# Kernel tuning notes

Measured on AMD Instinct MI355X. Metric: run time of the kernel, lower is better.

The kernel has to match this reference:

```python
import jax, jax.numpy as jnp
import numpy as np

GAMMA = 0.01      # rbf gamma (init kwarg)
C = 10            # n_classes (len(nv))
NV = 500          # support vectors per class (equal segments)
# all (i, j) class pairs with i < j, in the original nested-loop order
PAIRS = np.array([(i, j) for i in range(C) for j in range(i + 1, C)], dtype=np.int32)
I_IDX = jnp.asarray(PAIRS[:, 0])  # [45]
J_IDX = jnp.asarray(PAIRS[:, 1])  # [45]


def setup_inputs() -> dict:
    key = jax.random.key(0)
    k1, k2, k3, k4 = jax.random.split(key, 4)
    x = jax.random.normal(k1, (8192, 256), dtype=jnp.float32)
    sv = jax.random.normal(k2, (5000, 256), dtype=jnp.float32)
    a = jax.random.normal(k3, (C - 1, 5000), dtype=jnp.float32) * 0.1  # dual coefs
    b = jax.random.normal(k4, (45,), dtype=jnp.float32) * 0.1          # intercepts per pair
    return {"x": x, "sv": sv, "a": a, "b": b}


def reference(x, sv, a, b):
    # RBF kernel matrix: k[n, s] = exp(-gamma * ||x_n - sv_s||^2)
    x_norm = jnp.sum(x * x, axis=1)[:, None]            # [N, 1]
    sv_norm = jnp.sum(sv * sv, axis=1)[None, :]         # [1, SV]
    k = jnp.exp(-GAMMA * (x_norm + sv_norm) + 2.0 * GAMMA * (x @ sv.T))  # [N, SV]

    N = x.shape[0]
    kr = k.reshape(N, C, NV)           # per-class SV segments
    ar = a.reshape(C - 1, C, NV)       # dual coef rows, segmented the same way
    # T[n, r, c] = sum_m a[r, segment c, m] * k[n, segment c, m]
    # (fuses every inner Python loop of the original into one contraction)
    T = jnp.einsum('ncm,rcm->nrc', kr, ar)              # [N, C-1, C]

    # decision for pair (i, j): a[i, seg j] . k_seg_j + a[j-1, seg i] . k_seg_i + b
    c = T[:, I_IDX, J_IDX] + T[:, J_IDX - 1, I_IDX] + b[None, :]  # [N, 45]

    # pairwise voting: winner i if c > 0 else j; class id = mode of votes
    votes = jnp.where(c > 0, I_IDX[None, :], J_IDX[None, :])      # [N, 45] int32
    counts = jnp.sum(jax.nn.one_hot(votes, C, dtype=jnp.float32), axis=1)  # [N, C]
    # argmax picks the smallest class index on ties, matching torch.mode
    class_ids = jnp.argmax(counts, axis=1).astype(jnp.int32)
    return (class_ids, class_ids)
```

## Files before the change

### kernel.cpp

```cpp
#include <hip/hip_runtime.h>
#include <hip/hip_fp16.h>
#include <cmath>


#define GAMMA 0.01f
constexpr int N  = 8192;
constexpr int D  = 256;
constexpr int S  = 5000;
constexpr int C  = 10;
constexpr int NV = 500;
constexpr int R  = 9;
constexpr int SPAD = 5120;

constexpr int ROW_BLOCKS = (N + S) / 4;
constexpr int A_BLOCKS   = (16 * SPAD) / 256;

typedef _Float16 f16x8 __attribute__((ext_vector_type(8)));
typedef _Float16 f16x4 __attribute__((ext_vector_type(4)));
typedef float    f32x4 __attribute__((ext_vector_type(4)));

__device__ __forceinline__ void gload16(const void* g, void* l) {
    __builtin_amdgcn_global_load_lds(
        (const __attribute__((address_space(1))) void*)g,
        (__attribute__((address_space(3))) void*)l, 16, 0, 0);
}

__global__ __launch_bounds__(256) void prep_kernel(const float* __restrict__ x,
                                                   const float* __restrict__ sv,
                                                   const float* __restrict__ a,
                                                   _Float16* __restrict__ xth,
                                                   _Float16* __restrict__ xtl,
                                                   _Float16* __restrict__ sh,
                                                   _Float16* __restrict__ sl,
                                                   float* __restrict__ xn,
                                                   _Float16* __restrict__ ah,
                                                   _Float16* __restrict__ al,
                                                   float* __restrict__ svnp) {
    if (blockIdx.x >= ROW_BLOCKS) {
        int idx = (blockIdx.x - ROW_BLOCKS) * 256 + threadIdx.x;
        int r = idx / SPAD, col = idx - r * SPAD;
        int cls = col >> 9, j = col & 511;
        int s = cls * NV + ((j < NV) ? j : NV - 1);
        float av = (r < R && j < NV) ? a[(size_t)r * S + s] : 0.0f;
        _Float16 h = (_Float16)av;
        ah[idx] = h;
        al[idx] = (_Float16)((av - (float)h) * 4096.0f);
        return;
    }
    int gid  = blockIdx.x * blockDim.x + threadIdx.x;
    int wid  = gid >> 6;
    int lane = gid & 63;
    bool isx = wid < N;
    int  r   = isx ? wid : wid - N;
    const float* row = isx ? (x + (size_t)r * D) : (sv + (size_t)r * D);
    float4 v = reinterpret_cast<const float4*>(row)[lane];
    float s = v.x * v.x + v.y * v.y + v.z * v.z + v.w * v.w;
#pragma unroll
    for (int off = 32; off > 0; off >>= 1) s += __shfl_xor(s, off, 64);
    float vv[4] = {v.x, v.y, v.z, v.w};
    f16x4 h, l;
#pragma unroll
    for (int k = 0; k < 4; ++k) {
        _Float16 hi = (_Float16)vv[k];
        h[k] = hi;
        l[k] = (_Float16)((vv[k] - (float)hi) * 4096.0f);
    }
    if (isx) {
        size_t xt = (((size_t)(r >> 4) * 8 + (lane >> 3)) * 4 + ((lane >> 1) & 3)) * 128
                  + (size_t)(r & 15) * 8 + (lane & 1) * 4;
        *(f16x4*)(xth + xt) = h;
        *(f16x4*)(xtl + xt) = l;
    } else {
        size_t o = (size_t)r * D + lane * 4;
        *(f16x4*)(sh + o) = h;
        *(f16x4*)(sl + o) = l;
    }
    if (lane == 0) {
        if (isx) {
            xn[r] = s;
        } else {
            int cls = r / NV, j = r - cls * NV;
            svnp[cls * 512 + j] = s;
            if (j == NV - 1)
                for (int p = NV; p < 512; ++p) svnp[cls * 512 + p] = s;
        }
    }
}

__global__ __launch_bounds__(128, 3) void svc_gemm(const _Float16* __restrict__ xth,
                                                   const _Float16* __restrict__ xtl,
                                                   const _Float16* __restrict__ sh,
                                                   const _Float16* __restrict__ sl,
                                                   const _Float16* __restrict__ ahp,
                                                   const _Float16* __restrict__ alp,
                                                   const float* __restrict__ xnorm,
                                                   const float* __restrict__ svnp,
                                                   float* __restrict__ T) {
    __shared__ _Float16 SVs[2][2][64 * 32];

    const int tid  = threadIdx.x;
    const int n0   = blockIdx.x * 64;
    const int cls  = blockIdx.y;
    const int w    = tid >> 6;
    const int lane = tid & 63;
    const int lx   = lane & 15;
    const int quad = lane >> 4;

    float xnr[2];
#pragma unroll
    for (int nt = 0; nt < 2; ++nt)
        xnr[nt] = xnorm[n0 + w * 32 + nt * 16 + lx];

    int svoff[4];
#pragma unroll
    for (int mt = 0; mt < 4; ++mt) {
        int row = mt * 16 + lx;
        svoff[mt] = row * 32 + ((quad - (row >> 1)) & 3) * 8;
    }

    const int arow = tid >> 2, ag = tid & 3;
    const int sg   = (ag + (arow >> 1)) & 3;
    const int segend = cls * NV + NV - 1;
    const int ldsw = w * 512;

    auto stage = [&](int ph, int buf) {
        const int ch = ph >> 3, kb = ph & 7;
        const size_t koff = (size_t)(kb * 32 + sg * 8);
        const int svbase = cls * NV + ch * 64;
        int svr0 = svbase + arow;      if (svr0 > segend) svr0 = segend;
        int svr1 = svbase + arow + 32; if (svr1 > segend) svr1 = segend;
        const size_t go0 = (size_t)svr0 * D + koff;
        const size_t go1 = (size_t)svr1 * D + koff;
        gload16(sh + go0, &SVs[buf][0][ldsw]);
        gload16(sl + go0, &SVs[buf][1][ldsw]);
        gload16(sh + go1, &SVs[buf][0][1024 + ldsw]);
        gload16(sl + go1, &SVs[buf][1][1024 + ldsw]);
    };

    const int pn0 = blockIdx.x * 4 + w * 2;
    const size_t xq = (size_t)quad * 128 + (size_t)lx * 8;
    f16x8 pBE[2][2], pBO[2][2];
    auto loadB = [&](f16x8 (&dst)[2][2], int kb) {
        const size_t o0 = ((size_t)(pn0 * 8 + kb) * 4) * 128 + xq;
        const size_t o1 = ((size_t)((pn0 + 1) * 8 + kb) * 4) * 128 + xq;
        dst[0][0] = *(const f16x8*)(xth + o0);
        dst[1][0] = *(const f16x8*)(xtl + o0);
        dst[0][1] = *(const f16x8*)(xth + o1);
        dst[1][1] = *(const f16x8*)(xtl + o1);
    };

    f32x4 accM[4][2], accC[4][2];
#pragma unroll
    for (int mt = 0; mt < 4; ++mt)
#pragma unroll
        for (int nt = 0; nt < 2; ++nt) {
            accM[mt][nt] = (f32x4){0.f, 0.f, 0.f, 0.f};
            accC[mt][nt] = (f32x4){0.f, 0.f, 0.f, 0.f};
        }
    f32x4 accO[2], accOC[2];
#pragma unroll
    for (int nt = 0; nt < 2; ++nt) {
        accO[nt]  = (f32x4){0.f, 0.f, 0.f, 0.f};
        accOC[nt] = (f32x4){0.f, 0.f, 0.f, 0.f};
    }

    auto compute = [&](int buf, const f16x8 (&pB)[2][2]) {
        f16x8 Am[2][4];
#pragma unroll
        for (int mt = 0; mt < 4; ++mt) {
            Am[0][mt] = *(const f16x8*)(&SVs[buf][0][svoff[mt]]);
            Am[1][mt] = *(const f16x8*)(&SVs[buf][1][svoff[mt]]);
        }
        __builtin_amdgcn_s_setprio(1);
#pragma unroll
        for (int mt = 0; mt < 4; ++mt)
#pragma unroll
            for (int nt = 0; nt < 2; ++nt) {
                accM[mt][nt] = __builtin_amdgcn_mfma_f32_16x16x32_f16(
                    Am[0][mt], pB[0][nt], accM[mt][nt], 0, 0, 0);
                accC[mt][nt] = __builtin_amdgcn_mfma_f32_16x16x32_f16(
                    Am[0][mt], pB[1][nt], accC[mt][nt], 0, 0, 0);
                accC[mt][nt] = __builtin_amdgcn_mfma_f32_16x16x32_f16(
                    Am[1][mt], pB[0][nt], accC[mt][nt], 0, 0, 0);
            }
        __builtin_amdgcn_s_setprio(0);
    };

    auto epilogue = [&](int ch) {
        const int mbase = cls * 512 + ch * 64;
#pragma unroll
        for (int mt = 0; mt < 4; ++mt) {
            const size_t ao = (size_t)lx * SPAD + mbase + mt * 16 + quad * 4;
            f16x4 afh = *(const f16x4*)(ahp + ao);
            f16x4 afl = *(const f16x4*)(alp + ao);
            float4 sn4 = *(const float4*)(svnp + mbase + mt * 16 + quad * 4);
#pragma unroll
            for (int nt = 0; nt < 2; ++nt) {
                f16x4 bh, bl;
#pragma unroll
                for (int reg = 0; reg < 4; ++reg) {
                    float dot = accM[mt][nt][reg]
                              + accC[mt][nt][reg] * (1.0f / 4096.0f);
                    float e  = fmaf(2.0f * GAMMA, dot,
                                    -GAMMA * (xnr[nt] + sn4[reg]));
                    float kv = __expf(e);
                    _Float16 h = (_Float16)kv;
                    bh[reg] = h;
                    bl[reg] = (_Float16)((kv - (float)h) * 4096.0f);
                }
                accO[nt]  = __builtin_amdgcn_mfma_f32_16x16x16f16(
                    afh, bh, accO[nt], 0, 0, 0);
                accOC[nt] = __builtin_amdgcn_mfma_f32_16x16x16f16(
                    afh, bl, accOC[nt], 0, 0, 0);
                accOC[nt] = __builtin_amdgcn_mfma_f32_16x16x16f16(
                    afl, bh, accOC[nt], 0, 0, 0);
                accM[mt][nt] = (f32x4){0.f, 0.f, 0.f, 0.f};
                accC[mt][nt] = (f32x4){0.f, 0.f, 0.f, 0.f};
            }
        }
    };

    stage(0, 0);
    loadB(pBE, 0);

    for (int it = 0; it < 32; ++it) {
        asm volatile("s_waitcnt lgkmcnt(0)" ::: "memory");
        asm volatile("s_waitcnt vmcnt(4)" ::: "memory");
        __builtin_amdgcn_s_barrier();
        asm volatile("" ::: "memory");
        stage(2 * it + 1, 1);
        loadB(pBO, (2 * it + 1) & 7);
        compute(0, pBE);
        asm volatile("s_waitcnt lgkmcnt(0)" ::: "memory");
        asm volatile("s_waitcnt vmcnt(4)" ::: "memory");
        __builtin_amdgcn_s_barrier();
        asm volatile("" ::: "memory");
        if (it < 31) {
            stage(2 * it + 2, 0);
            loadB(pBE, (2 * it + 2) & 7);
        }
        compute(1, pBO);
        if ((it & 3) == 3) epilogue(it >> 2);
    }

#pragma unroll
    for (int nt = 0; nt < 2; ++nt)
#pragma unroll
        for (int reg = 0; reg < 4; ++reg) {
            int r = quad * 4 + reg;
            if (r < R) {
                int n = n0 + w * 32 + nt * 16 + lx;
                T[(size_t)(r * 10 + cls) * N + n] =
                    accO[nt][reg] + accOC[nt][reg] * (1.0f / 4096.0f);
            }
        }
}

__global__ __launch_bounds__(256) void vote_kernel(const float* __restrict__ T,
                                                   const float* __restrict__ b,
                                                   int* __restrict__ out) {
    int n = blockIdx.x * blockDim.x + threadIdx.x;
    if (n >= N) return;
    float tv[90];
#pragma unroll
    for (int i = 0; i < 90; ++i) tv[i] = T[(size_t)i * N + n];
    int counts[C];
#pragma unroll
    for (int k = 0; k < C; ++k) counts[k] = 0;
    int p = 0;
#pragma unroll
    for (int i = 0; i < C; ++i) {
#pragma unroll
        for (int j = i + 1; j < C; ++j) {
            float c = tv[i * 10 + j] + tv[(j - 1) * 10 + i] + b[p];
            if (c > 0.f) counts[i]++; else counts[j]++;
            ++p;
        }
    }
    int best = 0;
#pragma unroll
    for (int k = 1; k < C; ++k)
        if (counts[k] > counts[best]) best = k;
    out[n]     = best;
    out[N + n] = best;
}

extern "C" void kernel_launch(void* const* d_in, const int* in_sizes, int n_in,
                              void* d_out, int out_size, void* d_ws, size_t ws_size,
                              hipStream_t stream) {
    const float* x  = (const float*)d_in[0];
    const float* sv = (const float*)d_in[1];
    const float* a  = (const float*)d_in[2];
    const float* b  = (const float*)d_in[3];
    int* out = (int*)d_out;

    char* wp = (char*)d_ws;
    _Float16* xth = (_Float16*)wp; wp += (size_t)N * D * 2;
    _Float16* xtl = (_Float16*)wp; wp += (size_t)N * D * 2;
    _Float16* sh  = (_Float16*)wp; wp += (size_t)S * D * 2;
    _Float16* sl  = (_Float16*)wp; wp += (size_t)S * D * 2;
    float* xnorm  = (float*)wp;    wp += (size_t)N * 4;
    _Float16* ahp = (_Float16*)wp; wp += (size_t)16 * SPAD * 2;
    _Float16* alp = (_Float16*)wp; wp += (size_t)16 * SPAD * 2;
    float* svnp   = (float*)wp;    wp += (size_t)SPAD * 4;
    float* T      = (float*)wp;

    {
        prep_kernel<<<ROW_BLOCKS + A_BLOCKS, 256, 0, stream>>>(
            x, sv, a, xth, xtl, sh, sl, xnorm, ahp, alp, svnp);
    }
    {
        dim3 grid(N / 64, C);
        svc_gemm<<<grid, 128, 0, stream>>>(xth, xtl, sh, sl, ahp, alp,
                                           xnorm, svnp, T);
    }
    {
        vote_kernel<<<N / 256, 256, 0, stream>>>(T, b, out);
    }
}
```

Measured before the change: 169.9 us.

## Use single-wave GEMM blocks to drop barriers in the pipelined loop

Shrinks each svc_gemm block to one 64-lane wave covering 32 rows, so the LDS double-buffer no longer needs s_barrier between phases and relies only on vmcnt/lgkmcnt waits. The wave now issues all eight SV tile loads itself, and the grid doubles. This removes cross-wave synchronisation stalls at the cost of loading each SV tile twice as often from global/L2 memory.

```diff
diff --git a/kernel.cpp b/kernel.cpp
--- a/kernel.cpp
+++ b/kernel.cpp
@@ -87,29 +87,27 @@
     }
 }
 
-__global__ __launch_bounds__(128, 3) void svc_gemm(const _Float16* __restrict__ xth,
-                                                   const _Float16* __restrict__ xtl,
-                                                   const _Float16* __restrict__ sh,
-                                                   const _Float16* __restrict__ sl,
-                                                   const _Float16* __restrict__ ahp,
-                                                   const _Float16* __restrict__ alp,
-                                                   const float* __restrict__ xnorm,
-                                                   const float* __restrict__ svnp,
-                                                   float* __restrict__ T) {
+__global__ __launch_bounds__(64, 3) void svc_gemm(const _Float16* __restrict__ xth,
+                                                  const _Float16* __restrict__ xtl,
+                                                  const _Float16* __restrict__ sh,
+                                                  const _Float16* __restrict__ sl,
+                                                  const _Float16* __restrict__ ahp,
+                                                  const _Float16* __restrict__ alp,
+                                                  const float* __restrict__ xnorm,
+                                                  const float* __restrict__ svnp,
+                                                  float* __restrict__ T) {
     __shared__ _Float16 SVs[2][2][64 * 32];
 
-    const int tid  = threadIdx.x;
-    const int n0   = blockIdx.x * 64;
+    const int lane = threadIdx.x;
+    const int n0   = blockIdx.x * 32;
     const int cls  = blockIdx.y;
-    const int w    = tid >> 6;
-    const int lane = tid & 63;
     const int lx   = lane & 15;
     const int quad = lane >> 4;
 
     float xnr[2];
 #pragma unroll
     for (int nt = 0; nt < 2; ++nt)
-        xnr[nt] = xnorm[n0 + w * 32 + nt * 16 + lx];
+        xnr[nt] = xnorm[n0 + nt * 16 + lx];
 
     int svoff[4];
 #pragma unroll
@@ -118,26 +116,25 @@
         svoff[mt] = row * 32 + ((quad - (row >> 1)) & 3) * 8;
     }
 
-    const int arow = tid >> 2, ag = tid & 3;
-    const int sg   = (ag + (arow >> 1)) & 3;
     const int segend = cls * NV + NV - 1;
-    const int ldsw = w * 512;
+    const int svbase0 = cls * NV;
 
     auto stage = [&](int ph, int buf) {
         const int ch = ph >> 3, kb = ph & 7;
-        const size_t koff = (size_t)(kb * 32 + sg * 8);
-        const int svbase = cls * NV + ch * 64;
-        int svr0 = svbase + arow;      if (svr0 > segend) svr0 = segend;
-        int svr1 = svbase + arow + 32; if (svr1 > segend) svr1 = segend;
-        const size_t go0 = (size_t)svr0 * D + koff;
-        const size_t go1 = (size_t)svr1 * D + koff;
-        gload16(sh + go0, &SVs[buf][0][ldsw]);
-        gload16(sl + go0, &SVs[buf][1][ldsw]);
-        gload16(sh + go1, &SVs[buf][0][1024 + ldsw]);
-        gload16(sl + go1, &SVs[buf][1][1024 + ldsw]);
+#pragma unroll
+        for (int j = 0; j < 8; ++j) {
+            const int pl = j & 1, rg = j >> 1;
+            const int rl = rg * 16 + (lane >> 2);
+            const int sg = ((lane & 3) + (rl >> 1)) & 3;
+            int svr = svbase0 + ch * 64 + rl;
+            if (svr > segend) svr = segend;
+            const size_t go = (size_t)svr * D + kb * 32 + sg * 8;
+            gload16((pl ? sl : sh) + go,
+                    &SVs[buf][pl][rg * 512 + lane * 8]);
+        }
     };
 
-    const int pn0 = blockIdx.x * 4 + w * 2;
+    const int pn0 = blockIdx.x * 2;
     const size_t xq = (size_t)quad * 128 + (size_t)lx * 8;
     f16x8 pBE[2][2], pBO[2][2];
     auto loadB = [&](f16x8 (&dst)[2][2], int kb) {
@@ -225,20 +222,20 @@
 
     for (int it = 0; it < 32; ++it) {
         asm volatile("s_waitcnt lgkmcnt(0)" ::: "memory");
-        asm volatile("s_waitcnt vmcnt(4)" ::: "memory");
-        __builtin_amdgcn_s_barrier();
-        asm volatile("" ::: "memory");
         stage(2 * it + 1, 1);
         loadB(pBO, (2 * it + 1) & 7);
+        asm volatile("s_waitcnt vmcnt(12)" ::: "memory");
+        asm volatile("" ::: "memory");
         compute(0, pBE);
         asm volatile("s_waitcnt lgkmcnt(0)" ::: "memory");
-        asm volatile("s_waitcnt vmcnt(4)" ::: "memory");
-        __builtin_amdgcn_s_barrier();
-        asm volatile("" ::: "memory");
         if (it < 31) {
             stage(2 * it + 2, 0);
             loadB(pBE, (2 * it + 2) & 7);
-        }
+            asm volatile("s_waitcnt vmcnt(12)" ::: "memory");
+        } else {
+            asm volatile("s_waitcnt vmcnt(0)" ::: "memory");
+        }
+        asm volatile("" ::: "memory");
         compute(1, pBO);
         if ((it & 3) == 3) epilogue(it >> 2);
     }
@@ -249,7 +246,7 @@
         for (int reg = 0; reg < 4; ++reg) {
             int r = quad * 4 + reg;
             if (r < R) {
-                int n = n0 + w * 32 + nt * 16 + lx;
+                int n = n0 + nt * 16 + lx;
                 T[(size_t)(r * 10 + cls) * N + n] =
                     accO[nt][reg] + accOC[nt][reg] * (1.0f / 4096.0f);
             }
@@ -310,9 +307,9 @@
             x, sv, a, xth, xtl, sh, sl, xnorm, ahp, alp, svnp);
     }
     {
-        dim3 grid(N / 64, C);
-        svc_gemm<<<grid, 128, 0, stream>>>(xth, xtl, sh, sl, ahp, alp,
-                                           xnorm, svnp, T);
+        dim3 grid(N / 32, C);
+        svc_gemm<<<grid, 64, 0, stream>>>(xth, xtl, sh, sl, ahp, alp,
+                                          xnorm, svnp, T);
     }
     {
         vote_kernel<<<N / 256, 256, 0, stream>>>(T, b, out);
```

Result: slower. 219.6 us (+29.3%).
